# Kernel optimization log

Hardware: AMD Instinct MI355X
Metric: run time of the kernel (lower is better)

Reference implementation:

```python
import jax, jax.numpy as jnp
import numpy as np

B, S, D, H = 2, 2048, 1024, 16
DK = D // H  # 64
NEG_FILL = -1e-08  # faithful to the original (NOT -1e9)


def setup_inputs() -> dict:
    key = jax.random.key(0)
    ks = jax.random.split(key, 11)
    init = 1.0 / np.sqrt(D)
    inp = {
        "Q": jax.random.normal(ks[0], (B, S, D), jnp.float32),
        "K": jax.random.normal(ks[1], (B, S, D), jnp.float32),
        "V": jax.random.normal(ks[2], (B, S, D), jnp.float32),
        # causal mask, broadcast over batch and heads
        "mask": jnp.tril(jnp.ones((1, 1, S, S), jnp.int32)),
        "Wq": jax.random.normal(ks[3], (D, D), jnp.float32) * init,
        "bq": jnp.zeros((D,), jnp.float32),
        "Wk": jax.random.normal(ks[4], (D, D), jnp.float32) * init,
        "bk": jnp.zeros((D,), jnp.float32),
        "Wv": jax.random.normal(ks[5], (D, D), jnp.float32) * init,
        "bv": jnp.zeros((D,), jnp.float32),
        "Wo": jax.random.normal(ks[6], (D, D), jnp.float32) * init,
        "bo": jnp.zeros((D,), jnp.float32),
    }
    return inp


def reference(Q, K, V, mask, Wq, bq, Wk, bk, Wv, bv, Wo, bo):
    # Linear projections (weights stored as [in, out]; same math as nn.Linear)
    q = Q @ Wq + bq  # [B,S,D]
    k = K @ Wk + bk
    v = V @ Wv + bv
    # split heads: [B,S,D] -> [B,H,S,DK]
    q = q.reshape(B, S, H, DK).transpose(0, 2, 1, 3)
    k = k.reshape(B, S, H, DK).transpose(0, 2, 1, 3)
    v = v.reshape(B, S, H, DK).transpose(0, 2, 1, 3)
    scores = jnp.einsum("bhqd,bhkd->bhqk", q, k) / np.sqrt(DK)  # [B,H,S,S]
    scores = jnp.where(mask == 0, NEG_FILL, scores)
    probs = jax.nn.softmax(scores, axis=-1)
    # dropout p=0.0 -> identity (deterministic baseline)
    ctx = jnp.einsum("bhqk,bhkd->bhqd", probs, v)  # [B,H,S,DK]
    ctx = ctx.transpose(0, 2, 1, 3).reshape(B, S, D)
    return ctx @ Wo + bo
```

## Files before the change

kernel.cpp:

```cpp
#include <hip/hip_runtime.h>
#include <hip/hip_bf16.h>
#include <stdint.h>
#include <math.h>

#define DI __device__ __forceinline__

typedef __bf16 bf16x8 __attribute__((ext_vector_type(8)));
typedef float f32x4 __attribute__((ext_vector_type(4)));
typedef unsigned short ushortx8 __attribute__((ext_vector_type(8)));

DI unsigned short f2bf(float f) {
    unsigned int u = __builtin_bit_cast(unsigned int, f);
    u += 0x7fffu + ((u >> 16) & 1u);
    return (unsigned short)(u >> 16);
}

DI unsigned int cvt_pk_bf16(float lo, float hi) {
    unsigned int r;
    asm("v_cvt_pk_bf16_f32 %0, %1, %2" : "=v"(r) : "v"(lo), "v"(hi));
    return r;
}

DI f32x4 mfma_16x16x32_bf16(bf16x8 a, bf16x8 b, f32x4 c) {
    return __builtin_amdgcn_mfma_f32_16x16x32_bf16(a, b, c, 0, 0, 0);
}

DI void gload16(const unsigned short* g, unsigned short* l) {
    __builtin_amdgcn_global_load_lds(
        (const __attribute__((address_space(1))) void*)g,
        (__attribute__((address_space(3))) void*)l, 16, 0, 0);
}

__global__ __launch_bounds__(256) void k_prep(
    const float* __restrict__ Q, const float* __restrict__ K, const float* __restrict__ V,
    unsigned short* __restrict__ qc, unsigned short* __restrict__ kc, unsigned short* __restrict__ vc,
    const float* __restrict__ w0, const float* __restrict__ w1,
    const float* __restrict__ w2, const float* __restrict__ w3,
    unsigned short* __restrict__ o0, unsigned short* __restrict__ o1,
    unsigned short* __restrict__ o2, unsigned short* __restrict__ o3)
{
    constexpr int N = 1024;
    __shared__ unsigned short L[64 * 64];
    const int bx = blockIdx.x;
    const int tid = threadIdx.x;

    if (bx < 3072) {
        const int z = bx >> 10;
        const int ib = bx & 1023;
        const float* s = z == 0 ? Q : z == 1 ? K : V;
        unsigned short* d = z == 0 ? qc : z == 1 ? kc : vc;
        const int i0 = ib * 256 + tid;
        #pragma unroll
        for (int it = 0; it < 4; ++it) {
            const int i = i0 + it * 262144;
            const float4 v = reinterpret_cast<const float4*>(s)[i];
            uint2 pk;
            pk.x = cvt_pk_bf16(v.x, v.y);
            pk.y = cvt_pk_bf16(v.z, v.w);
            reinterpret_cast<uint2*>(d)[i] = pk;
        }
    } else {
        const int r4 = bx - 3072;
        const int z = r4 >> 8;
        const int tile = r4 & 255;
        const float* W = z == 0 ? w0 : z == 1 ? w1 : z == 2 ? w2 : w3;
        unsigned short* O = z == 0 ? o0 : z == 1 ? o1 : z == 2 ? o2 : o3;
        const int k0 = (tile >> 4) * 64, n0 = (tile & 15) * 64;

        const int r = tid >> 2, cbase = (tid & 3) * 16;
        #pragma unroll
        for (int i = 0; i < 4; ++i) {
            const int c = cbase + i * 4;
            const float4 v = *reinterpret_cast<const float4*>(&W[(size_t)(k0 + r) * N + n0 + c]);
            uint2 pk;
            pk.x = cvt_pk_bf16(v.x, v.y);
            pk.y = cvt_pk_bf16(v.z, v.w);
            const int byte = r * 128 + ((c * 2) ^ ((r & 7) << 4));
            *reinterpret_cast<uint2*>(reinterpret_cast<char*>(L) + byte) = pk;
        }
        __syncthreads();

        const int n = tid >> 2, kc2 = (tid & 3) * 16;
        ushortx8 v0, v1;
        #pragma unroll
        for (int j = 0; j < 8; ++j) {
            const int ka = kc2 + j, kb2 = kc2 + 8 + j;
            v0[j] = *reinterpret_cast<const unsigned short*>(
                reinterpret_cast<const char*>(L) + ka * 128 + ((n * 2) ^ ((ka & 7) << 4)));
            v1[j] = *reinterpret_cast<const unsigned short*>(
                reinterpret_cast<const char*>(L) + kb2 * 128 + ((n * 2) ^ ((kb2 & 7) << 4)));
        }
        unsigned short* op = &O[(size_t)(n0 + n) * N + k0 + kc2];
        *reinterpret_cast<ushortx8*>(op) = v0;
        *reinterpret_cast<ushortx8*>(op + 8) = v1;
    }
}

template <int MODE, int BN>
__global__ __launch_bounds__(256) void k_gemm_bf16(
    const unsigned short* __restrict__ A0, const unsigned short* __restrict__ A1,
    const unsigned short* __restrict__ A2,
    const unsigned short* __restrict__ B0, const unsigned short* __restrict__ B1,
    const unsigned short* __restrict__ B2,
    const float* __restrict__ bias0, const float* __restrict__ bias1,
    const float* __restrict__ bias2,
    void* C0, void* C1, void* C2)
{
    constexpr int K = 1024, N = 1024;
    constexpr int NJ = BN / 32;
    const int z = MODE ? blockIdx.z : 0;
    const unsigned short* A  = z == 0 ? A0 : z == 1 ? A1 : A2;
    const unsigned short* Bt = z == 0 ? B0 : z == 1 ? B1 : B2;
    const float* bias        = z == 0 ? bias0 : z == 1 ? bias1 : bias2;
    void* C                  = z == 0 ? C0 : z == 1 ? C1 : C2;

    __shared__ unsigned short As[128 * 64];
    __shared__ unsigned short Bs[BN * 64];

    const int tid  = threadIdx.x;
    const int lane = tid & 63;
    const int w    = tid >> 6;
    const int wr   = w >> 1, wc = w & 1;
    const int fr   = lane & 15, kg = lane >> 4;
    const int m0   = blockIdx.x * 128, n0 = blockIdx.y * BN;

    const int srow8 = lane >> 3;
    const int sswz  = ((lane & 7) ^ (lane >> 3)) * 8;

    f32x4 acc[4][NJ] = {};

    for (int t = 0; t < K / 64; ++t) {
        const int k0 = t * 64;
        #pragma unroll
        for (int it = 0; it < 4; ++it) {
            const int c = w * 4 + it;
            gload16(&A[(size_t)(m0 + c * 8 + srow8) * K + k0 + sswz], &As[c * 512]);
            if (BN == 128)
                gload16(&Bt[(size_t)(n0 + c * 8 + srow8) * K + k0 + sswz], &Bs[c * 512]);
        }
        if (BN == 64) {
            #pragma unroll
            for (int it = 0; it < 2; ++it) {
                const int c = w * 2 + it;
                gload16(&Bt[(size_t)(n0 + c * 8 + srow8) * K + k0 + sswz], &Bs[c * 512]);
            }
        }
        __syncthreads();

        const int rsw = (fr & 7) << 4;
        #pragma unroll
        for (int kh = 0; kh < 2; ++kh) {
            bf16x8 af[4], bfj[NJ];
            #pragma unroll
            for (int i = 0; i < 4; ++i)
                af[i] = *reinterpret_cast<const bf16x8*>(
                    reinterpret_cast<const char*>(As) +
                    (wr * 64 + i * 16 + fr) * 128 + ((kh * 64 + kg * 16) ^ rsw));
            #pragma unroll
            for (int j = 0; j < NJ; ++j)
                bfj[j] = *reinterpret_cast<const bf16x8*>(
                    reinterpret_cast<const char*>(Bs) +
                    (wc * (BN / 2) + j * 16 + fr) * 128 + ((kh * 64 + kg * 16) ^ rsw));
            #pragma unroll
            for (int i = 0; i < 4; ++i)
                #pragma unroll
                for (int j = 0; j < NJ; ++j)
                    acc[i][j] = mfma_16x16x32_bf16(af[i], bfj[j], acc[i][j]);
        }
        __syncthreads();
    }

    if (MODE == 1 && z == 2) {
        unsigned short* vt = reinterpret_cast<unsigned short*>(C);
        #pragma unroll
        for (int i = 0; i < 4; ++i) {
            const int m = m0 + wr * 64 + i * 16 + kg * 4;
            const int bb = m >> 11, s = m & 2047;
            #pragma unroll
            for (int j = 0; j < NJ; ++j) {
                const int n = n0 + wc * (BN / 2) + j * 16 + fr;
                const float bv = bias[n];
                uint2 pk;
                pk.x = cvt_pk_bf16(acc[i][j][0] + bv, acc[i][j][1] + bv);
                pk.y = cvt_pk_bf16(acc[i][j][2] + bv, acc[i][j][3] + bv);
                *reinterpret_cast<uint2*>(&vt[((size_t)(bb * 1024 + n)) * 2048 + s]) = pk;
            }
        }
    } else if (MODE == 1) {
        const float sc = (z == 0) ? 0.125f * 1.44269504088896340736f : 1.0f;
        unsigned short* Cb = reinterpret_cast<unsigned short*>(C);
        #pragma unroll
        for (int i = 0; i < 4; ++i) {
            const int m = m0 + wr * 64 + i * 16 + kg * 4;
            #pragma unroll
            for (int j = 0; j < NJ; ++j) {
                const int n = n0 + wc * (BN / 2) + j * 16 + fr;
                const float bv = bias[n];
                const unsigned int p0 = cvt_pk_bf16((acc[i][j][0] + bv) * sc, (acc[i][j][1] + bv) * sc);
                const unsigned int p1 = cvt_pk_bf16((acc[i][j][2] + bv) * sc, (acc[i][j][3] + bv) * sc);
                Cb[(size_t)(m + 0) * N + n] = (unsigned short)p0;
                Cb[(size_t)(m + 1) * N + n] = (unsigned short)(p0 >> 16);
                Cb[(size_t)(m + 2) * N + n] = (unsigned short)p1;
                Cb[(size_t)(m + 3) * N + n] = (unsigned short)(p1 >> 16);
            }
        }
    } else {
        float* Cf = reinterpret_cast<float*>(C);
        #pragma unroll
        for (int i = 0; i < 4; ++i) {
            const int m = m0 + wr * 64 + i * 16 + kg * 4;
            #pragma unroll
            for (int j = 0; j < NJ; ++j) {
                const int n = n0 + wc * (BN / 2) + j * 16 + fr;
                const float bv = bias[n];
                #pragma unroll
                for (int r = 0; r < 4; ++r)
                    Cf[(size_t)(m + r) * N + n] = acc[i][j][r] + bv;
            }
        }
    }
}

__global__ __launch_bounds__(256) void k_vtail(
    const unsigned short* __restrict__ vt, float* __restrict__ vtail)
{
    const int row = blockIdx.x * 4 + (threadIdx.x >> 6);
    const int l = threadIdx.x & 63;
    const unsigned short* p = &vt[(size_t)row * 2048 + l * 32];
    float s = 0.f;
    #pragma unroll
    for (int i = 0; i < 4; ++i) {
        ushortx8 v = *reinterpret_cast<const ushortx8*>(&p[i * 8]);
        #pragma unroll
        for (int e = 0; e < 8; ++e)
            s += __builtin_bit_cast(float, (unsigned int)v[e] << 16);
    }
    #pragma unroll
    for (int off = 1; off < 64; off <<= 1) {
        const float t = __shfl_down(s, off, 64);
        s += (l + off < 64) ? t : 0.f;
    }
    float tv = __shfl(s, (2 * l + 2) & 63, 64);
    if (l == 31) tv = 0.f;
    if (l < 32) vtail[(size_t)row * 32 + l] = tv;
}

template <bool MASK>
DI void attn_tile(const unsigned char* KsB, const unsigned char* VtsB,
                  unsigned char* PB, bf16x8 qf0, bf16x8 qf1,
                  f32x4 (&o)[4], f32x4& oS, int w, int fr, int kg)
{
    const int sw = (fr & 7) << 4;
    #pragma unroll
    for (int j = 0; j < 4; ++j) {
        const int row = j * 16 + fr;
        const bf16x8 kf0 = *reinterpret_cast<const bf16x8*>(KsB + row * 128 + ((kg * 16) ^ sw));
        const bf16x8 kf1 = *reinterpret_cast<const bf16x8*>(KsB + row * 128 + ((64 + kg * 16) ^ sw));
        f32x4 s = {0.f, 0.f, 0.f, 0.f};
        __builtin_amdgcn_s_setprio(1);
        s = mfma_16x16x32_bf16(kf0, qf0, s);
        s = mfma_16x16x32_bf16(kf1, qf1, s);
        __builtin_amdgcn_s_setprio(0);
        float p[4];
        #pragma unroll
        for (int r = 0; r < 4; ++r) {
            float e = __builtin_amdgcn_exp2f(s[r]);
            if (MASK && (j * 16 + kg * 4 + r > w * 16 + fr)) e = 1.0f;
            p[r] = e;
        }
        uint2 pk;
        pk.x = cvt_pk_bf16(p[0], p[1]);
        pk.y = cvt_pk_bf16(p[2], p[3]);
        *reinterpret_cast<uint2*>(PB + fr * 128 + ((j * 32 + kg * 8) ^ sw)) = pk;
    }
    bf16x8 ones;
    #pragma unroll
    for (int b = 0; b < 8; ++b) ones[b] = (__bf16)1.0f;
    __builtin_amdgcn_s_setprio(1);
    #pragma unroll
    for (int kk = 0; kk < 2; ++kk) {
        const bf16x8 pf = *reinterpret_cast<const bf16x8*>(PB + fr * 128 + ((kk * 64 + kg * 16) ^ sw));
        #pragma unroll
        for (int n = 0; n < 4; ++n) {
            const int vrow = n * 16 + fr;
            const bf16x8 vf = *reinterpret_cast<const bf16x8*>(VtsB + vrow * 128 + ((kk * 64 + kg * 16) ^ sw));
            o[n] = mfma_16x16x32_bf16(pf, vf, o[n]);
        }
        oS = mfma_16x16x32_bf16(pf, ones, oS);
    }
    __builtin_amdgcn_s_setprio(0);
}

DI void attn_sweep(int qt,
                   const unsigned short* __restrict__ qp,
                   const unsigned short* __restrict__ kp,
                   const unsigned short* __restrict__ vt,
                   const float* __restrict__ vtail,
                   unsigned short* __restrict__ ctx,
                   unsigned char (*KsB)[64 * 128], unsigned char (*VtsB)[64 * 128],
                   unsigned char* PB, size_t baseQ, size_t baseV, int b, int h,
                   int lane, int w, int fr, int kg)
{
    constexpr int S = 2048, D = 1024;
    const int q0 = qt * 64 + w * 16;

    bf16x8 qf0, qf1;
    {
        const size_t roff = baseQ + (size_t)(q0 + fr) * D;
        qf0 = *reinterpret_cast<const bf16x8*>(&qp[roff + kg * 8]);
        qf1 = *reinterpret_cast<const bf16x8*>(&qp[roff + 32 + kg * 8]);
    }

    f32x4 o[4] = {};
    f32x4 oS = {};
    const int NT = qt + 1;

    const int srow = lane >> 3;
    const int sswz = ((lane & 7) ^ srow) * 8;
    const int c0   = w * 2;

    #pragma unroll
    for (int i = 0; i < 2; ++i) {
        const int c = c0 + i;
        const int row = c * 8 + srow;
        gload16(&kp[baseQ + (size_t)row * D + sswz],
                reinterpret_cast<unsigned short*>(KsB[0] + c * 1024));
        gload16(&vt[baseV + (size_t)row * S + sswz],
                reinterpret_cast<unsigned short*>(VtsB[0] + c * 1024));
    }
    __syncthreads();

    for (int t = 0; t < NT; ++t) {
        const int cur = t & 1;
        if (t + 1 < NT) {
            const int kt1 = (t + 1) * 64;
            #pragma unroll
            for (int i = 0; i < 2; ++i) {
                const int c = c0 + i;
                const int row = c * 8 + srow;
                gload16(&kp[baseQ + (size_t)(kt1 + row) * D + sswz],
                        reinterpret_cast<unsigned short*>(KsB[cur ^ 1] + c * 1024));
                gload16(&vt[baseV + (size_t)row * S + kt1 + sswz],
                        reinterpret_cast<unsigned short*>(VtsB[cur ^ 1] + c * 1024));
            }
        }
        if (t == NT - 1)
            attn_tile<true>(KsB[cur], VtsB[cur], PB, qf0, qf1, o, oS, w, fr, kg);
        else
            attn_tile<false>(KsB[cur], VtsB[cur], PB, qf0, qf1, o, oS, w, fr, kg);
        __syncthreads();
    }

    const float tailc = (float)(S - (qt + 1) * 64);
    float rlq[4];
    #pragma unroll
    for (int r = 0; r < 4; ++r) rlq[r] = 1.0f / (oS[r] + tailc);

    float tl[4];
    #pragma unroll
    for (int n = 0; n < 4; ++n)
        tl[n] = vtail[((size_t)(b * 1024) + h * 64 + n * 16 + fr) * 32 + qt];

    #pragma unroll
    for (int n = 0; n < 4; ++n)
        #pragma unroll
        for (int r = 0; r < 4; ++r) {
            const int qrow = q0 + kg * 4 + r;
            ctx[baseQ + (size_t)qrow * D + n * 16 + fr] = f2bf((o[n][r] + tl[n]) * rlq[r]);
        }
}

__global__ __launch_bounds__(256, 2) void k_attn(
    const unsigned short* __restrict__ qp,
    const unsigned short* __restrict__ kp,
    const unsigned short* __restrict__ vt,
    const float* __restrict__ vtail,
    unsigned short* __restrict__ ctx)
{
    constexpr int S = 2048, D = 1024;
    const int L = blockIdx.x;
    const int G = (L & 7) * 64 + (L >> 3);
    const int p = G & 15;
    const int h = (G >> 4) & 15;
    const int b = G >> 8;

    __shared__ alignas(16) unsigned char KsB[2][64 * 128];
    __shared__ alignas(16) unsigned char VtsB[2][64 * 128];
    __shared__ alignas(16) unsigned char PlsB[4 * 16 * 128];

    const int tid  = threadIdx.x;
    const int lane = tid & 63, w = tid >> 6;
    const int fr   = lane & 15, kg = lane >> 4;
    unsigned char* PB = PlsB + w * 2048;

    const size_t baseQ = ((size_t)b * S) * D + (size_t)h * 64;
    const size_t baseV = ((size_t)b * D + (size_t)h * 64) * S;

    attn_sweep(31 - p, qp, kp, vt, vtail, ctx, KsB, VtsB, PB,
               baseQ, baseV, b, h, lane, w, fr, kg);
    attn_sweep(p, qp, kp, vt, vtail, ctx, KsB, VtsB, PB,
               baseQ, baseV, b, h, lane, w, fr, kg);
}

extern "C" void kernel_launch(void* const* d_in, const int* in_sizes, int n_in,
                              void* d_out, int out_size, void* d_ws, size_t ws_size,
                              hipStream_t stream) {
    constexpr int B = 2, S = 2048, D = 1024;
    constexpr int M = B * S;
    constexpr size_t MD = (size_t)M * D;

    const float* Q  = (const float*)d_in[0];
    const float* K  = (const float*)d_in[1];
    const float* V  = (const float*)d_in[2];
    const float* Wq = (const float*)d_in[4];
    const float* bq = (const float*)d_in[5];
    const float* Wk = (const float*)d_in[6];
    const float* bk = (const float*)d_in[7];
    const float* Wv = (const float*)d_in[8];
    const float* bv = (const float*)d_in[9];
    const float* Wo = (const float*)d_in[10];
    const float* bo = (const float*)d_in[11];

    unsigned short* qc = (unsigned short*)d_out;
    unsigned short* kc = qc + MD;
    char* ws = (char*)d_ws;
    unsigned short* qb  = (unsigned short*)(ws);
    unsigned short* kb  = (unsigned short*)(ws + (8u << 20));
    unsigned short* vtg = (unsigned short*)(ws + (16u << 20));
    unsigned short* vc  = (unsigned short*)(ws + (24u << 20));
    unsigned short* Wto = (unsigned short*)(ws + (32u << 20));
    unsigned short* Wtq = (unsigned short*)(ws + (34u << 20));
    unsigned short* Wtk = (unsigned short*)(ws + (36u << 20));
    unsigned short* Wtv = (unsigned short*)(ws + (38u << 20));
    unsigned short* ctx = vc;
    float* vtail        = (float*)Wtq;

    dim3 blk(256);
    k_prep<<<dim3(4096), blk, 0, stream>>>(
        Q, K, V, qc, kc, vc, Wq, Wk, Wv, Wo, Wtq, Wtk, Wtv, Wto);
    k_gemm_bf16<1, 64><<<dim3(M / 128, D / 64, 3), blk, 0, stream>>>(
        qc, kc, vc, Wtq, Wtk, Wtv, bq, bk, bv, qb, kb, vtg);
    k_vtail<<<dim3((B * D) / 4), blk, 0, stream>>>(vtg, vtail);
    k_attn<<<dim3(512), blk, 0, stream>>>(qb, kb, vtg, vtail, ctx);
    k_gemm_bf16<0, 64><<<dim3(M / 128, D / 64, 1), blk, 0, stream>>>(
        ctx, ctx, ctx, Wto, Wto, Wto, bo, bo, bo, d_out, d_out, d_out);
}
```

Measured before the change: 117.8 us.

## Triple-buffer K/V tiles with prefetch depth two and partial vmcnt waits

Moves the attention sweep from double-buffered to triple-buffered shared memory for the K and V^T tiles. Each iteration issues loads two tiles ahead and waits with s_waitcnt vmcnt(4), so only the next tile's loads must be complete, followed by a raw s_barrier. The goal is to hide more global-load latency behind the MFMA work. In exchange, LDS use rises by 16KB per block, which could limit the two-blocks-per-CU occupancy. The correctness of the vmcnt counts also depends on gload16 being async LDS loads that the vmcnt counter tracks.

```diff
diff --git a/kernel.cpp b/kernel.cpp
--- a/kernel.cpp
+++ b/kernel.cpp
@@ -319,37 +319,44 @@
     const int sswz = ((lane & 7) ^ srow) * 8;
     const int c0   = w * 2;
 
-    #pragma unroll
-    for (int i = 0; i < 2; ++i) {
-        const int c = c0 + i;
-        const int row = c * 8 + srow;
-        gload16(&kp[baseQ + (size_t)row * D + sswz],
-                reinterpret_cast<unsigned short*>(KsB[0] + c * 1024));
-        gload16(&vt[baseV + (size_t)row * S + sswz],
-                reinterpret_cast<unsigned short*>(VtsB[0] + c * 1024));
-    }
-    __syncthreads();
+    #define STAGE_DMA(TT, BUF)                                                   \
+        {                                                                        \
+            const int kb_ = (TT) * 64;                                           \
+            _Pragma("unroll")                                                    \
+            for (int i_ = 0; i_ < 2; ++i_) {                                     \
+                const int c_ = c0 + i_;                                          \
+                const int row_ = c_ * 8 + srow;                                  \
+                gload16(&kp[baseQ + (size_t)(kb_ + row_) * D + sswz],            \
+                        reinterpret_cast<unsigned short*>(KsB[BUF] + c_ * 1024));\
+                gload16(&vt[baseV + (size_t)row_ * S + kb_ + sswz],              \
+                        reinterpret_cast<unsigned short*>(VtsB[BUF] + c_ * 1024));\
+            }                                                                    \
+        }
+
+    STAGE_DMA(0, 0);
+    if (NT > 1) {
+        STAGE_DMA(1, 1);
+        asm volatile("s_waitcnt vmcnt(4)" ::: "memory");
+    } else {
+        asm volatile("s_waitcnt vmcnt(0)" ::: "memory");
+    }
+    __builtin_amdgcn_s_barrier();
 
     for (int t = 0; t < NT; ++t) {
-        const int cur = t & 1;
-        if (t + 1 < NT) {
-            const int kt1 = (t + 1) * 64;
-            #pragma unroll
-            for (int i = 0; i < 2; ++i) {
-                const int c = c0 + i;
-                const int row = c * 8 + srow;
-                gload16(&kp[baseQ + (size_t)(kt1 + row) * D + sswz],
-                        reinterpret_cast<unsigned short*>(KsB[cur ^ 1] + c * 1024));
-                gload16(&vt[baseV + (size_t)row * S + kt1 + sswz],
-                        reinterpret_cast<unsigned short*>(VtsB[cur ^ 1] + c * 1024));
-            }
-        }
+        const int cur = t % 3;
+        const bool has2 = (t + 2 < NT);
+        if (has2) STAGE_DMA(t + 2, (t + 2) % 3);
         if (t == NT - 1)
             attn_tile<true>(KsB[cur], VtsB[cur], PB, qf0, qf1, o, oS, w, fr, kg);
         else
             attn_tile<false>(KsB[cur], VtsB[cur], PB, qf0, qf1, o, oS, w, fr, kg);
-        __syncthreads();
-    }
+        if (t + 1 < NT) {
+            if (has2) asm volatile("s_waitcnt vmcnt(4)" ::: "memory");
+            else      asm volatile("s_waitcnt vmcnt(0)" ::: "memory");
+            __builtin_amdgcn_s_barrier();
+        }
+    }
+    #undef STAGE_DMA
 
     const float tailc = (float)(S - (qt + 1) * 64);
     float rlq[4];
@@ -368,6 +375,8 @@
             const int qrow = q0 + kg * 4 + r;
             ctx[baseQ + (size_t)qrow * D + n * 16 + fr] = f2bf((o[n][r] + tl[n]) * rlq[r]);
         }
+
+    __syncthreads();
 }
 
 __global__ __launch_bounds__(256, 2) void k_attn(
@@ -384,8 +393,8 @@
     const int h = (G >> 4) & 15;
     const int b = G >> 8;
 
-    __shared__ alignas(16) unsigned char KsB[2][64 * 128];
-    __shared__ alignas(16) unsigned char VtsB[2][64 * 128];
+    __shared__ alignas(16) unsigned char KsB[3][64 * 128];
+    __shared__ alignas(16) unsigned char VtsB[3][64 * 128];
     __shared__ alignas(16) unsigned char PlsB[4 * 16 * 128];
 
     const int tid  = threadIdx.x;
```

Result: no change. 115.6 us, median of 2 (-1.9%).
